# Performance work log

Measured on AMD Instinct MI355X. Metric: run time of the kernel, lower is better.

Reference implementation:

```python
import jax, jax.numpy as jnp
import numpy as np

B, IN, H, D, C, K = 4096, 128, 256, 32, 8, 256
HS = D // 2  # structure_filter hidden (latent_dim > 2)
EPS = 1e-6
MAX_NORM = 0.99


def _gelu(t):
    return jax.nn.gelu(t, approximate=False)  # torch nn.GELU default = exact erf


def _project_to_ball(z):
    norm = jnp.maximum(jnp.linalg.norm(z, axis=-1, keepdims=True), EPS)
    scale = jnp.minimum(MAX_NORM / norm, 1.0)
    return z * scale


def _hyperbolic_distance(xp, yp):
    # Poincare-ball distance: arccosh(1 + 2*|x-y|^2 / ((1-|x|^2)(1-|y|^2)))
    sq = jnp.sum((xp - yp) ** 2, axis=-1)
    xn = jnp.sum(xp * xp, axis=-1)
    yn = jnp.sum(yp * yp, axis=-1)
    denom = jnp.maximum((1.0 - xn) * (1.0 - yn), EPS)
    arg = jnp.maximum(1.0 + 2.0 * sq / denom, 1.0 + EPS)
    return jnp.arccosh(arg)


def setup_inputs() -> dict:
    key = jax.random.key(0)
    ks = jax.random.split(key, 14)
    n = lambda k, shape, s: (jax.random.normal(k, shape, dtype=jnp.float32) * s)
    centers = jax.random.normal(ks[7], (C, D), dtype=jnp.float32)
    centers = centers / jnp.maximum(jnp.linalg.norm(centers, axis=-1, keepdims=True), EPS)
    return {
        "x": jax.random.normal(ks[0], (B, IN), dtype=jnp.float32),
        "W1": n(ks[1], (IN, H), 0.05), "b1": jnp.zeros((H,), jnp.float32),
        "W2": n(ks[2], (H, H), 0.05), "b2": jnp.zeros((H,), jnp.float32),
        "Wv": n(ks[3], (H, D), 0.05), "bv": jnp.zeros((D,), jnp.float32),
        "centers": centers,
        "codebook": n(ks[8], (C, K, D), 0.02),
        "Ws1": n(ks[9], (D, HS), 0.1), "bs1": jnp.zeros((HS,), jnp.float32),
        "Ws2": n(ks[10], (HS, D), 0.1), "bs2": jnp.zeros((D,), jnp.float32),
    }


def reference(x, W1, b1, W2, b2, Wv, bv, centers, codebook, Ws1, bs1, Ws2, bs2):
    sg = jax.lax.stop_gradient
    feats = _gelu(_gelu(x @ W1 + b1) @ W2 + b2)          # [B,H]
    v = feats @ Wv + bv                                   # [B,D]
    scores = (v @ centers.T) / jnp.sqrt(jnp.asarray(D, v.dtype))
    router = jax.nn.softmax(scores, axis=-1)              # [B,C]
    K_chart = jnp.argmax(router, axis=1)                  # [B]
    c_bar = router @ centers                              # [B,D]
    v_local = v - c_bar                                   # [B,D]
    diff = v_local[:, None, None, :] - codebook[None]     # [B,C,K,D]
    dist = jnp.sum(diff * diff, axis=-1)                  # [B,C,K]
    indices = jnp.argmin(dist, axis=-1)                   # [B,C]
    z_q_all = codebook[jnp.arange(C)[None, :], indices]   # [B,C,D]
    v_bc = jnp.broadcast_to(v_local[:, None, :], z_q_all.shape)
    v_proj = _project_to_ball(v_bc)
    w_det = sg(router)
    d_cb = _hyperbolic_distance(z_q_all, sg(v_proj))      # [B,C]
    codebook_loss = jnp.sum(jnp.mean(d_cb ** 2 * w_det, axis=0))
    d_cm = _hyperbolic_distance(sg(z_q_all), v_proj)
    commitment = jnp.sum(jnp.mean(d_cm ** 2 * w_det, axis=0))
    vq_loss = codebook_loss + 0.25 * commitment
    z_q_blended = jnp.sum(z_q_all * router[..., None], axis=1)  # [B,D]
    K_code = jnp.take_along_axis(indices, K_chart[:, None], axis=1)[:, 0]
    delta = v_local[:, None, :] - sg(z_q_all)             # [B,C,D]
    z_n_all = _gelu(delta @ Ws1 + bs1) @ Ws2 + bs2        # [B,C,D]
    z_n = jnp.sum(z_n_all * router[..., None], axis=1)    # [B,D]
    z_tex = (v_local - sg(z_q_blended)) - z_n
    z_q_st = v_local + sg(z_q_blended - v_local)
    z_geo = c_bar + z_q_st + z_n
    return (K_chart, K_code, z_n, z_tex, router, z_geo, vq_loss, indices, z_n_all, c_bar, v_local)
```

## Files before the change

### kernel.cpp

```cpp
#include <hip/hip_runtime.h>
#include <math.h>

#define NB 4096
#define NIN 128
#define NH 256
#define ND 32
#define NC 8
#define NK 256
#define NHS 16

#define OFF_KCHART 0
#define OFF_KCODE  4096
#define OFF_ZN     8192
#define OFF_ZTEX   (OFF_ZN + 4096*32)
#define OFF_ROUTER (OFF_ZTEX + 4096*32)
#define OFF_ZGEO   (OFF_ROUTER + 4096*8)
#define OFF_LOSS   (OFF_ZGEO + 4096*32)
#define OFF_IND    (OFF_LOSS + 1)
#define OFF_ZNALL  (OFF_IND + 4096*8)
#define OFF_CBAR   (OFF_ZNALL + 4096*8*32)
#define OFF_VLOC   (OFF_CBAR + 4096*32)

__device__ __forceinline__ float gelu_exact(float x) {
    return x * (erff(x / 1.41421356237309504f) + 1.0f) * 0.5f;
}

template<int K>
__global__ __launch_bounds__(256)
void gemm_bias_gelu(const float* __restrict__ A, const float* __restrict__ W,
                    const float* __restrict__ bias, float* __restrict__ out) {
    const int N = 256;
    __shared__ float sB[2][32][68];
    const int t  = threadIdx.x;
    const int n0 = blockIdx.x * 64;
    const int r0 = blockIdx.y * 32;
    const int ty = t >> 4, tx = t & 15;
    const int bk = t >> 4, bc = t & 15;

    float4 bias4 = *(const float4*)(bias + n0 + tx * 4);

    float4 pb0 = *(const float4*)(W + bk * N + n0 + bc * 4);
    float4 pb1 = *(const float4*)(W + (bk + 16) * N + n0 + bc * 4);

    const float* Ab0 = A + (r0 + ty * 2 + 0) * K;
    const float* Ab1 = A + (r0 + ty * 2 + 1) * K;
    float ac[2][4], an[2][4];
    {
        float4 c0 = *(const float4*)(Ab0 + 0), c1 = *(const float4*)(Ab1 + 0);
        ac[0][0]=c0.x; ac[0][1]=c0.y; ac[0][2]=c0.z; ac[0][3]=c0.w;
        ac[1][0]=c1.x; ac[1][1]=c1.y; ac[1][2]=c1.z; ac[1][3]=c1.w;
        float4 d0 = *(const float4*)(Ab0 + 4), d1 = *(const float4*)(Ab1 + 4);
        an[0][0]=d0.x; an[0][1]=d0.y; an[0][2]=d0.z; an[0][3]=d0.w;
        an[1][0]=d1.x; an[1][1]=d1.y; an[1][2]=d1.z; an[1][3]=d1.w;
    }

    float acc[2][4];
    #pragma unroll
    for (int i = 0; i < 2; i++)
        #pragma unroll
        for (int j = 0; j < 4; j++) acc[i][j] = 0.f;

    int buf = 0;
    for (int kk = 0; kk < K; kk += 32) {
        *(float4*)(&sB[buf][bk][bc*4])    = pb0;
        *(float4*)(&sB[buf][bk+16][bc*4]) = pb1;
        __syncthreads();
        if (kk + 32 < K) {
            pb0 = *(const float4*)(W + (kk + 32 + bk) * N + n0 + bc * 4);
            pb1 = *(const float4*)(W + (kk + 32 + bk + 16) * N + n0 + bc * 4);
        }
        #pragma unroll
        for (int c = 0; c < 8; c++) {
            int knext = kk + (c + 2) * 4;
            if (knext > K - 4) knext = K - 4;
            float4 p0 = *(const float4*)(Ab0 + knext);
            float4 p1 = *(const float4*)(Ab1 + knext);
            #pragma unroll
            for (int u = 0; u < 4; u++) {
                float4 bv = *(const float4*)(&sB[buf][c * 4 + u][tx * 4]);
                float bb[4] = {bv.x, bv.y, bv.z, bv.w};
                #pragma unroll
                for (int j = 0; j < 4; j++) {
                    acc[0][j] = fmaf(ac[0][u], bb[j], acc[0][j]);
                    acc[1][j] = fmaf(ac[1][u], bb[j], acc[1][j]);
                }
            }
            #pragma unroll
            for (int u = 0; u < 4; u++) { ac[0][u] = an[0][u]; ac[1][u] = an[1][u]; }
            an[0][0]=p0.x; an[0][1]=p0.y; an[0][2]=p0.z; an[0][3]=p0.w;
            an[1][0]=p1.x; an[1][1]=p1.y; an[1][2]=p1.z; an[1][3]=p1.w;
        }
        buf ^= 1;
    }
    float bb4[4] = {bias4.x, bias4.y, bias4.z, bias4.w};
    #pragma unroll
    for (int i = 0; i < 2; i++) {
        int row = r0 + ty * 2 + i;
        float4 o;
        float* op = (float*)&o;
        #pragma unroll
        for (int j = 0; j < 4; j++) op[j] = gelu_exact(acc[i][j] + bb4[j]);
        *(float4*)(out + row * N + n0 + tx * 4) = o;
    }
}

__global__ __launch_bounds__(256)
void router_kernel(const float* __restrict__ feats, const float* __restrict__ Wv,
                   const float* __restrict__ bv, const float* __restrict__ centers,
                   float* __restrict__ out, float* __restrict__ vloc_ws) {
    __shared__ float sWv[32 * 272];
    __shared__ float sCent[NC * ND];
    __shared__ float sV[8][ND + 2];
    __shared__ float sScore[8][NC];
    __shared__ float sRout[8][NC];
    const int t = threadIdx.x;
    const int row0 = blockIdx.x * 8;
    {
        #pragma unroll
        for (int q = 0; q < 8; q++) {
            int id = t + q * 256;
            int k = id >> 3, c4 = (id & 7) * 4;
            int kb = k >> 2, kr = k & 3;
            float4 w = ((const float4*)Wv)[id];
            sWv[(c4+0) * 272 + ((kb ^ ((c4+0) & 7)) << 2) + kr] = w.x;
            sWv[(c4+1) * 272 + ((kb ^ ((c4+1) & 7)) << 2) + kr] = w.y;
            sWv[(c4+2) * 272 + ((kb ^ ((c4+2) & 7)) << 2) + kr] = w.z;
            sWv[(c4+3) * 272 + ((kb ^ ((c4+3) & 7)) << 2) + kr] = w.w;
        }
        if (t < 64) ((float4*)sCent)[t] = ((const float4*)centers)[t];
    }
    __syncthreads();
    const int r = t >> 5, cp = t & 31;
    const int row = row0 + r;
    const int cbase = cp * 272, cxor = cp & 7;
    float a0 = bv[cp];
    const float4* f4 = (const float4*)(feats + row * NH);
    for (int k4 = 0; k4 < NH / 4; k4++) {
        float4 f = f4[k4];
        float4 w = *(const float4*)(&sWv[cbase + ((k4 ^ cxor) << 2)]);
        a0 = fmaf(f.x, w.x, a0);
        a0 = fmaf(f.y, w.y, a0);
        a0 = fmaf(f.z, w.z, a0);
        a0 = fmaf(f.w, w.w, a0);
    }
    sV[r][cp] = a0;
    __syncthreads();
    if (t < 64) {
        int rr = t >> 3, c = t & 7;
        float s = 0.f;
        #pragma unroll
        for (int k = 0; k < ND; k++) s = fmaf(sV[rr][k], sCent[c * ND + k], s);
        sScore[rr][c] = s / 5.65685424949238f;
    }
    __syncthreads();
    if (t < 8) {
        const int rr = t, grow = row0 + rr;
        float sc[NC];
        float m = -3.4e38f; int kmax = 0;
        #pragma unroll
        for (int c = 0; c < NC; c++) {
            float s = sScore[rr][c];
            sc[c] = s;
            if (s > m) { m = s; kmax = c; }
        }
        float ssum = 0.f;
        #pragma unroll
        for (int c = 0; c < NC; c++) { float e = expf(sc[c] - m); sc[c] = e; ssum += e; }
        float inv = 1.f / ssum;
        #pragma unroll
        for (int c = 0; c < NC; c++) {
            float rv = sc[c] * inv;
            sRout[rr][c] = rv;
            out[OFF_ROUTER + grow * NC + c] = rv;
        }
        out[OFF_KCHART + grow] = (float)kmax;
    }
    __syncthreads();
    {
        const int col = cp;
        float cb = 0.f;
        #pragma unroll
        for (int c = 0; c < NC; c++) cb = fmaf(sRout[r][c], sCent[c * ND + col], cb);
        float vl = sV[r][col] - cb;
        out[OFF_CBAR + row * ND + col] = cb;
        out[OFF_VLOC + row * ND + col] = vl;
        vloc_ws[row * ND + col] = vl;
    }
}

__global__ __launch_bounds__(256, 2)
void vq_chart(const float* __restrict__ codebook, const float* __restrict__ vloc_ws,
              const float* __restrict__ Ws1, const float* __restrict__ bs1,
              const float* __restrict__ Ws2, const float* __restrict__ bs2,
              float* __restrict__ out, float* __restrict__ loss_partial) {
    __shared__ float sCB[NK][36];
    __shared__ float sEn2[NK];
    __shared__ float sV[64][36];
    __shared__ float sBest[16][64];
    __shared__ int   sBidx[16][64];
    __shared__ int   sSel[64];
    __shared__ float sRoutv[64];
    __shared__ float sPscale[64];
    __shared__ float sLossArr[64];
    __shared__ float sWs1T[NHS][36];
    __shared__ float sWs2T[ND][20];
    __shared__ float sbs1[NHS], sbs2v[ND];
    const int t = threadIdx.x;
    const int c = blockIdx.x & 7;
    const int row0 = (blockIdx.x >> 3) * 64;

    {
        const float4* src = (const float4*)(codebook + c * NK * ND);
        #pragma unroll
        for (int q = 0; q < 8; q++) {
            int id = t + q * 256;
            int code = id >> 3, kq = (id & 7) * 4;
            *(float4*)(&sCB[code][kq]) = src[id];
        }
        #pragma unroll
        for (int q = 0; q < 2; q++) {
            int id = t + q * 256;
            int rr = id >> 3, kq = (id & 7) * 4;
            *(float4*)(&sV[rr][kq]) = ((const float4*)(vloc_ws + row0 * ND))[id];
        }
    }
    if (t < 128) {
        float4 w = ((const float4*)Ws1)[t];
        int k = t >> 2, o = (t & 3) * 4;
        sWs1T[o+0][k] = w.x; sWs1T[o+1][k] = w.y;
        sWs1T[o+2][k] = w.z; sWs1T[o+3][k] = w.w;
    } else {
        int u = t - 128;
        float4 w = ((const float4*)Ws2)[u];
        int k = u >> 3, o = (u & 7) * 4;
        sWs2T[o+0][k] = w.x; sWs2T[o+1][k] = w.y;
        sWs2T[o+2][k] = w.z; sWs2T[o+3][k] = w.w;
    }
    if (t < NHS) sbs1[t] = bs1[t];
    else if (t < NHS + ND) sbs2v[t - NHS] = bs2[t - NHS];
    if (t < 64) sRoutv[t] = out[OFF_ROUTER + (row0 + t) * NC + c];
    __syncthreads();
    {
        float s = 0.f;
        #pragma unroll
        for (int q = 0; q < 8; q++) {
            float4 e = *(const float4*)(&sCB[t][q * 4]);
            s = fmaf(e.x, e.x, s); s = fmaf(e.y, e.y, s);
            s = fmaf(e.z, e.z, s); s = fmaf(e.w, e.w, s);
        }
        sEn2[t] = s;
    }
    __syncthreads();

    {
        const int r = t & 15, g = t >> 4;
        float vl[4][ND];
        #pragma unroll
        for (int u = 0; u < 4; u++) {
            #pragma unroll
            for (int q = 0; q < 8; q++) {
                float4 a = *(const float4*)(&sV[r + u * 16][q * 4]);
                vl[u][q*4] = a.x; vl[u][q*4+1] = a.y;
                vl[u][q*4+2] = a.z; vl[u][q*4+3] = a.w;
            }
        }
        float best[4] = {3.4e38f, 3.4e38f, 3.4e38f, 3.4e38f};
        int bi[4] = {0, 0, 0, 0};
        for (int j = 0; j < 16; j++) {
            const int code = g * 16 + ((j + g * 4) & 15);
            float dot[4] = {0.f, 0.f, 0.f, 0.f};
            #pragma unroll
            for (int q = 0; q < 8; q++) {
                float4 e = *(const float4*)(&sCB[code][q * 4]);
                #pragma unroll
                for (int u = 0; u < 4; u++) {
                    dot[u] = fmaf(vl[u][q*4+0], e.x, dot[u]);
                    dot[u] = fmaf(vl[u][q*4+1], e.y, dot[u]);
                    dot[u] = fmaf(vl[u][q*4+2], e.z, dot[u]);
                    dot[u] = fmaf(vl[u][q*4+3], e.w, dot[u]);
                }
            }
            const float en2 = sEn2[code];
            #pragma unroll
            for (int u = 0; u < 4; u++) {
                float d = en2 - 2.f * dot[u];
                if (d < best[u] || (d == best[u] && code < bi[u])) {
                    best[u] = d; bi[u] = code;
                }
            }
        }
        #pragma unroll
        for (int u = 0; u < 4; u++) {
            sBest[g][r + u * 16] = best[u];
            sBidx[g][r + u * 16] = bi[u];
        }
    }
    __syncthreads();
    if (t < 64) {
        float bb = sBest[0][t]; int ii = sBidx[0][t];
        #pragma unroll
        for (int gg = 1; gg < 16; gg++) {
            float v = sBest[gg][t]; int id = sBidx[gg][t];
            if (v < bb || (v == bb && id < ii)) { bb = v; ii = id; }
        }
        sSel[t] = ii;
        out[OFF_IND + (row0 + t) * NC + c] = (float)ii;
        float vn2 = 0.f;
        #pragma unroll
        for (int k = 0; k < ND; k++) { float v = sV[t][k]; vn2 = fmaf(v, v, vn2); }
        float norm = fmaxf(sqrtf(vn2), 1e-6f);
        sPscale[t] = fminf(0.99f / norm, 1.0f);
    }
    __syncthreads();

    const int i = t & 15, r16 = t >> 4;
    const float b1r = sbs1[i];
    const float bo0 = sbs2v[2*i], bo1 = sbs2v[2*i+1];
    float w1c[ND], w2a[NHS], w2b[NHS];
    #pragma unroll
    for (int q = 0; q < 8; q++) {
        float4 w = *(const float4*)(&sWs1T[i][q * 4]);
        w1c[q*4] = w.x; w1c[q*4+1] = w.y; w1c[q*4+2] = w.z; w1c[q*4+3] = w.w;
    }
    #pragma unroll
    for (int q = 0; q < 4; q++) {
        float4 a = *(const float4*)(&sWs2T[2*i][q * 4]);
        w2a[q*4] = a.x; w2a[q*4+1] = a.y; w2a[q*4+2] = a.z; w2a[q*4+3] = a.w;
        float4 b = *(const float4*)(&sWs2T[2*i+1][q * 4]);
        w2b[q*4] = b.x; w2b[q*4+1] = b.y; w2b[q*4+2] = b.z; w2b[q*4+3] = b.w;
    }
    #pragma unroll
    for (int pass = 0; pass < 4; pass++) {
        const int lrow = pass * 16 + r16;
        const int grow = row0 + lrow;
        const int sel = sSel[lrow];
        const float rc = sRoutv[lrow];
        const float ps = sPscale[lrow];
        float dta[ND];
        #pragma unroll
        for (int q = 0; q < 8; q++) {
            float4 vv = *(const float4*)(&sV[lrow][q * 4]);
            float4 ee = *(const float4*)(&sCB[sel][q * 4]);
            dta[q*4+0] = vv.x - ee.x; dta[q*4+1] = vv.y - ee.y;
            dta[q*4+2] = vv.z - ee.z; dta[q*4+3] = vv.w - ee.w;
        }
        float acc1 = b1r;
        #pragma unroll
        for (int k = 0; k < ND; k++) acc1 = fmaf(dta[k], w1c[k], acc1);
        float h = gelu_exact(acc1);
        float a0 = bo0, a1 = bo1;
        #pragma unroll
        for (int k = 0; k < NHS; k++) {
            float s1k = __shfl(h, k, 16);
            a0 = fmaf(s1k, w2a[k], a0);
            a1 = fmaf(s1k, w2b[k], a1);
        }
        out[OFF_ZNALL + (grow * NC + c) * ND + 2*i]     = a0;
        out[OFF_ZNALL + (grow * NC + c) * ND + 2*i + 1] = a1;
        const float e0 = sCB[sel][2*i], e1 = sCB[sel][2*i+1];
        float yp0 = sV[lrow][2*i] * ps, yp1 = sV[lrow][2*i+1] * ps;
        float d0 = e0 - yp0, d1 = e1 - yp1;
        float sq = fmaf(d0, d0, d1 * d1);
        float xn = fmaf(e0, e0, e1 * e1);
        float yn = fmaf(yp0, yp0, yp1 * yp1);
        #pragma unroll
        for (int m = 1; m < 16; m <<= 1) {
            sq += __shfl_xor(sq, m, 16);
            xn += __shfl_xor(xn, m, 16);
            yn += __shfl_xor(yn, m, 16);
        }
        if (i == 0) {
            float denom = fmaxf((1.f - xn) * (1.f - yn), 1e-6f);
            float arg = fmaxf(1.f + 2.f * sq / denom, 1.f + 1e-6f);
            float dd = acoshf(arg);
            sLossArr[lrow] = dd * dd * rc;
        }
    }
    __syncthreads();
    if (t < 64) {
        float v = sLossArr[t];
        #pragma unroll
        for (int off = 32; off > 0; off >>= 1) v += __shfl_down(v, off, 64);
        if (t == 0) loss_partial[blockIdx.x] = v;
    }
}

__global__ __launch_bounds__(256)
void finalize2_kernel(const float* __restrict__ codebook, const float* __restrict__ vloc_ws,
                      float* __restrict__ out, const float* __restrict__ partials) {
    const int gid = blockIdx.x * 256 + threadIdx.x;
    const int row = gid >> 5;
    const int col = gid & 31;
    float rout[NC]; int ind[NC];
    #pragma unroll
    for (int cc = 0; cc < NC; cc++) {
        rout[cc] = out[OFF_ROUTER + row * NC + cc];
        ind[cc]  = (int)out[OFF_IND + row * NC + cc];
    }
    float zn = 0.f, zq = 0.f;
    #pragma unroll
    for (int cc = 0; cc < NC; cc++) {
        const float rcc = rout[cc];
        zn = fmaf(out[OFF_ZNALL + (row * NC + cc) * ND + col], rcc, zn);
        zq = fmaf(codebook[(cc * NK + ind[cc]) * ND + col], rcc, zq);
    }
    const float vl = vloc_ws[row * ND + col];
    const float cb = out[OFF_CBAR + row * ND + col];
    out[OFF_ZN   + row * ND + col] = zn;
    out[OFF_ZTEX + row * ND + col] = vl - zq - zn;
    out[OFF_ZGEO + row * ND + col] = cb + zq + zn;
    if (col == 0) {
        int kc = (int)out[OFF_KCHART + row];
        out[OFF_KCODE + row] = out[OFF_IND + row * NC + kc];
    }
    if (blockIdx.x == 0) {
        __shared__ float sTmp[4];
        const int t = threadIdx.x;
        float v = partials[t] + partials[t + 256];
        #pragma unroll
        for (int off = 32; off > 0; off >>= 1) v += __shfl_down(v, off, 64);
        if ((t & 63) == 0) sTmp[t >> 6] = v;
        __syncthreads();
        if (t == 0) out[OFF_LOSS] = 1.25f * (sTmp[0] + sTmp[1] + sTmp[2] + sTmp[3]) / 4096.f;
    }
}

extern "C" void kernel_launch(void* const* d_in, const int* in_sizes, int n_in,
                              void* d_out, int out_size, void* d_ws, size_t ws_size,
                              hipStream_t stream) {
    const float* x        = (const float*)d_in[0];
    const float* W1       = (const float*)d_in[1];
    const float* b1       = (const float*)d_in[2];
    const float* W2       = (const float*)d_in[3];
    const float* b2       = (const float*)d_in[4];
    const float* Wv       = (const float*)d_in[5];
    const float* bv       = (const float*)d_in[6];
    const float* centers  = (const float*)d_in[7];
    const float* codebook = (const float*)d_in[8];
    const float* Ws1      = (const float*)d_in[9];
    const float* bs1      = (const float*)d_in[10];
    const float* Ws2      = (const float*)d_in[11];
    const float* bs2      = (const float*)d_in[12];
    float* out = (float*)d_out;
    float* ws  = (float*)d_ws;

    float* h1       = ws;
    float* feats    = ws + 4096 * 256;
    float* vloc     = ws + 2 * 4096 * 256;
    float* partials = ws + 2 * 4096 * 256 + 4096 * 32;

    gemm_bias_gelu<128><<<dim3(4, 128), dim3(256), 0, stream>>>(x, W1, b1, h1);
    gemm_bias_gelu<256><<<dim3(4, 128), dim3(256), 0, stream>>>(h1, W2, b2, feats);
    router_kernel<<<dim3(512), dim3(256), 0, stream>>>(feats, Wv, bv, centers, out, vloc);
    vq_chart<<<dim3(512), dim3(256), 0, stream>>>(codebook, vloc, Ws1, bs1, Ws2, bs2, out, partials);
    finalize2_kernel<<<dim3(512), dim3(256), 0, stream>>>(codebook, vloc, out, partials);
}
```

Measured before the change: 60.44 us.

## Stream GEMM weights from global memory into registers instead of LDS tiles

Rewrites the two bias+GELU GEMM kernels to load W and A directly from global memory into double-buffered register sets, removing the shared-memory tile and block barriers. This aims to cut LDS traffic and synchronization overhead in the MLP stage. It relies on caches to serve the W reuse across threads and raises register usage and global load count.

```diff
diff --git a/kernel.cpp b/kernel.cpp
--- a/kernel.cpp
+++ b/kernel.cpp
@@ -25,73 +25,74 @@
     return x * (erff(x / 1.41421356237309504f) + 1.0f) * 0.5f;
 }
 
+#define GEMM_COMPUTE(AR0, AR1, BV)                                  \
+    {                                                               \
+        float ar0[8] = {AR0##a.x, AR0##a.y, AR0##a.z, AR0##a.w,     \
+                        AR0##b.x, AR0##b.y, AR0##b.z, AR0##b.w};    \
+        float ar1[8] = {AR1##a.x, AR1##a.y, AR1##a.z, AR1##a.w,     \
+                        AR1##b.x, AR1##b.y, AR1##b.z, AR1##b.w};    \
+        _Pragma("unroll")                                           \
+        for (int u = 0; u < 8; u++) {                               \
+            float bb[4] = {BV[u].x, BV[u].y, BV[u].z, BV[u].w};     \
+            _Pragma("unroll")                                       \
+            for (int j = 0; j < 4; j++) {                           \
+                acc[0][j] = fmaf(ar0[u], bb[j], acc[0][j]);         \
+                acc[1][j] = fmaf(ar1[u], bb[j], acc[1][j]);         \
+            }                                                       \
+        }                                                           \
+    }
+
 template<int K>
 __global__ __launch_bounds__(256)
-void gemm_bias_gelu(const float* __restrict__ A, const float* __restrict__ W,
-                    const float* __restrict__ bias, float* __restrict__ out) {
+void gemm_stream(const float* __restrict__ A, const float* __restrict__ W,
+                 const float* __restrict__ bias, float* __restrict__ out) {
     const int N = 256;
-    __shared__ float sB[2][32][68];
     const int t  = threadIdx.x;
     const int n0 = blockIdx.x * 64;
     const int r0 = blockIdx.y * 32;
     const int ty = t >> 4, tx = t & 15;
-    const int bk = t >> 4, bc = t & 15;
+
+    const float* Ar0 = A + (r0 + ty * 2 + 0) * K;
+    const float* Ar1 = A + (r0 + ty * 2 + 1) * K;
+    const float* Wb  = W + n0 + tx * 4;
 
     float4 bias4 = *(const float4*)(bias + n0 + tx * 4);
 
-    float4 pb0 = *(const float4*)(W + bk * N + n0 + bc * 4);
-    float4 pb1 = *(const float4*)(W + (bk + 16) * N + n0 + bc * 4);
-
-    const float* Ab0 = A + (r0 + ty * 2 + 0) * K;
-    const float* Ab1 = A + (r0 + ty * 2 + 1) * K;
-    float ac[2][4], an[2][4];
-    {
-        float4 c0 = *(const float4*)(Ab0 + 0), c1 = *(const float4*)(Ab1 + 0);
-        ac[0][0]=c0.x; ac[0][1]=c0.y; ac[0][2]=c0.z; ac[0][3]=c0.w;
-        ac[1][0]=c1.x; ac[1][1]=c1.y; ac[1][2]=c1.z; ac[1][3]=c1.w;
-        float4 d0 = *(const float4*)(Ab0 + 4), d1 = *(const float4*)(Ab1 + 4);
-        an[0][0]=d0.x; an[0][1]=d0.y; an[0][2]=d0.z; an[0][3]=d0.w;
-        an[1][0]=d1.x; an[1][1]=d1.y; an[1][2]=d1.z; an[1][3]=d1.w;
-    }
-
     float acc[2][4];
     #pragma unroll
     for (int i = 0; i < 2; i++)
         #pragma unroll
         for (int j = 0; j < 4; j++) acc[i][j] = 0.f;
 
-    int buf = 0;
-    for (int kk = 0; kk < K; kk += 32) {
-        *(float4*)(&sB[buf][bk][bc*4])    = pb0;
-        *(float4*)(&sB[buf][bk+16][bc*4]) = pb1;
-        __syncthreads();
-        if (kk + 32 < K) {
-            pb0 = *(const float4*)(W + (kk + 32 + bk) * N + n0 + bc * 4);
-            pb1 = *(const float4*)(W + (kk + 32 + bk + 16) * N + n0 + bc * 4);
-        }
-        #pragma unroll
-        for (int c = 0; c < 8; c++) {
-            int knext = kk + (c + 2) * 4;
-            if (knext > K - 4) knext = K - 4;
-            float4 p0 = *(const float4*)(Ab0 + knext);
-            float4 p1 = *(const float4*)(Ab1 + knext);
+    float4 xA0a = *(const float4*)(Ar0 + 0), xA0b = *(const float4*)(Ar0 + 4);
+    float4 xA1a = *(const float4*)(Ar1 + 0), xA1b = *(const float4*)(Ar1 + 4);
+    float4 xB[8];
+    #pragma unroll
+    for (int u = 0; u < 8; u++) xB[u] = *(const float4*)(Wb + u * N);
+
+    float4 yA0a, yA0b, yA1a, yA1b, yB[8];
+
+    #pragma unroll 4
+    for (int k0 = 0; k0 < K; k0 += 16) {
+        {
+            const int kn = k0 + 8;
+            yA0a = *(const float4*)(Ar0 + kn); yA0b = *(const float4*)(Ar0 + kn + 4);
+            yA1a = *(const float4*)(Ar1 + kn); yA1b = *(const float4*)(Ar1 + kn + 4);
             #pragma unroll
-            for (int u = 0; u < 4; u++) {
-                float4 bv = *(const float4*)(&sB[buf][c * 4 + u][tx * 4]);
-                float bb[4] = {bv.x, bv.y, bv.z, bv.w};
-                #pragma unroll
-                for (int j = 0; j < 4; j++) {
-                    acc[0][j] = fmaf(ac[0][u], bb[j], acc[0][j]);
-                    acc[1][j] = fmaf(ac[1][u], bb[j], acc[1][j]);
-                }
-            }
+            for (int u = 0; u < 8; u++) yB[u] = *(const float4*)(Wb + (kn + u) * N);
+        }
+        GEMM_COMPUTE(xA0, xA1, xB)
+        {
+            int kn = k0 + 16;
+            if (kn > K - 8) kn = K - 8;
+            xA0a = *(const float4*)(Ar0 + kn); xA0b = *(const float4*)(Ar0 + kn + 4);
+            xA1a = *(const float4*)(Ar1 + kn); xA1b = *(const float4*)(Ar1 + kn + 4);
             #pragma unroll
-            for (int u = 0; u < 4; u++) { ac[0][u] = an[0][u]; ac[1][u] = an[1][u]; }
-            an[0][0]=p0.x; an[0][1]=p0.y; an[0][2]=p0.z; an[0][3]=p0.w;
-            an[1][0]=p1.x; an[1][1]=p1.y; an[1][2]=p1.z; an[1][3]=p1.w;
-        }
-        buf ^= 1;
-    }
+            for (int u = 0; u < 8; u++) xB[u] = *(const float4*)(Wb + (kn + u) * N);
+        }
+        GEMM_COMPUTE(yA0, yA1, yB)
+    }
+
     float bb4[4] = {bias4.x, bias4.y, bias4.z, bias4.w};
     #pragma unroll
     for (int i = 0; i < 2; i++) {
@@ -449,8 +450,8 @@
     float* vloc     = ws + 2 * 4096 * 256;
     float* partials = ws + 2 * 4096 * 256 + 4096 * 32;
 
-    gemm_bias_gelu<128><<<dim3(4, 128), dim3(256), 0, stream>>>(x, W1, b1, h1);
-    gemm_bias_gelu<256><<<dim3(4, 128), dim3(256), 0, stream>>>(h1, W2, b2, feats);
+    gemm_stream<128><<<dim3(4, 128), dim3(256), 0, stream>>>(x, W1, b1, h1);
+    gemm_stream<256><<<dim3(4, 128), dim3(256), 0, stream>>>(h1, W2, b2, feats);
     router_kernel<<<dim3(512), dim3(256), 0, stream>>>(feats, Wv, bv, centers, out, vloc);
     vq_chart<<<dim3(512), dim3(256), 0, stream>>>(codebook, vloc, Ws1, bs1, Ws2, bs2, out, partials);
     finalize2_kernel<<<dim3(512), dim3(256), 0, stream>>>(codebook, vloc, out, partials);
```

Result: slower. 124.2 us (+105.5%).
